# Optimization experiments

Hardware: AMD Instinct MI355X
Metric: run time of the kernel (lower is better)

Reference implementation:

```python
import jax, jax.numpy as jnp
import numpy as np

N = 50000      # nodes
E = 800000     # edges
F_IN = 500     # input features
H = 128        # hidden_channels
C = 10         # classes


def setup_inputs() -> dict:
    key = jax.random.key(0)
    ks = jax.random.split(key, 9)
    x = jax.random.normal(ks[0], (N, F_IN), dtype=jnp.float32)
    edge_index = jax.random.randint(ks[1], (2, E), 0, N, dtype=jnp.int32)
    W1 = jax.random.normal(ks[2], (F_IN, H), dtype=jnp.float32) * 0.05
    b1 = jnp.zeros((H,), dtype=jnp.float32)
    W2 = jax.random.normal(ks[3], (H, H), dtype=jnp.float32) * 0.05
    b2 = jnp.zeros((H,), dtype=jnp.float32)
    Wo = jax.random.normal(ks[4], (H, C), dtype=jnp.float32) * 0.05
    bo = jnp.zeros((C,), dtype=jnp.float32)
    return {"x": x, "edge_index": edge_index, "W1": W1, "b1": b1,
            "W2": W2, "b2": b2, "Wo": Wo, "bo": bo}


def _gcn_conv(x, src, dst, norm, W, b):
    # x: [N, F] -> [N, out]; PyG GCNConv: transform, then normalized scatter-add
    h = x @ W                                    # [N, out]
    msg = h[src] * norm[:, None]                 # [E+N, out] gathered messages
    agg = jax.ops.segment_sum(msg, dst, num_segments=N)
    return agg + b


def reference(x, edge_index, W1, b1, W2, b2, Wo, bo):
    loop = jnp.arange(N, dtype=edge_index.dtype)
    src = jnp.concatenate([edge_index[0], loop])  # add self-loops
    dst = jnp.concatenate([edge_index[1], loop])
    # symmetric normalization deg^-1/2 A_hat deg^-1/2 (deg counted at target)
    deg = jnp.zeros((N,), dtype=x.dtype).at[dst].add(1.0)
    dis = jnp.where(deg > 0, jax.lax.rsqrt(deg), 0.0)
    norm = dis[src] * dis[dst]

    h = jax.nn.relu(_gcn_conv(x, src, dst, norm, W1, b1))
    h = jax.nn.relu(_gcn_conv(h, src, dst, norm, W2, b2))
    # eval-mode: dropout is identity
    return jax.nn.softmax(h @ Wo + bo, axis=1)
```

## Files before the change

### kernel.cpp

```cpp
#include <hip/hip_runtime.h>
#include <hip/hip_bf16.h>
#include <stdint.h>

#define N_NODES 50000
#define N_EDGES 800000
#define F_IN    500
#define HID     128
#define NCLS    10

typedef __attribute__((ext_vector_type(8))) short bf16x8;
typedef __attribute__((ext_vector_type(4))) float f32x4;

__device__ __forceinline__ float bf_lo(uint32_t u) { return __uint_as_float(u << 16); }
__device__ __forceinline__ float bf_hi(uint32_t u) { return __uint_as_float(u & 0xffff0000u); }
__device__ __forceinline__ uint32_t bf_pack(float a, float b) {
    __hip_bfloat162 t; t.x = __float2bfloat16(a); t.y = __float2bfloat16(b);
    uint32_t r; __builtin_memcpy(&r, &t, 4); return r;
}


__global__ __launch_bounds__(256) void count_deg_k(const int* __restrict__ dst, int* __restrict__ cnt) {
    int e = blockIdx.x * 256 + threadIdx.x;
    if (e < N_EDGES) atomicAdd(&cnt[dst[e]], 1);
}

__global__ __launch_bounds__(1024) void scan_dis_k(const int* __restrict__ cnt,
                                                   int* __restrict__ off,
                                                   float* __restrict__ dis) {
    __shared__ int part[1024];
    const int PER = 52;
    int tid = threadIdx.x;
    int base = tid * PER;
    int vals[PER];
    #pragma unroll
    for (int i = 0; i < PER; i += 4) {
        int idx = base + i;
        int4 v = make_int4(0, 0, 0, 0);
        if (idx + 3 < N_NODES) {
            v = *(const int4*)&cnt[idx];
        } else {
            if (idx + 0 < N_NODES) v.x = cnt[idx + 0];
            if (idx + 1 < N_NODES) v.y = cnt[idx + 1];
            if (idx + 2 < N_NODES) v.z = cnt[idx + 2];
            if (idx + 3 < N_NODES) v.w = cnt[idx + 3];
        }
        vals[i + 0] = v.x; vals[i + 1] = v.y; vals[i + 2] = v.z; vals[i + 3] = v.w;
    }
    int s = 0;
    #pragma unroll
    for (int i = 0; i < PER; ++i) s += vals[i];
    part[tid] = s;
    __syncthreads();
    for (int o = 1; o < 1024; o <<= 1) {
        int v = (tid >= o) ? part[tid - o] : 0;
        __syncthreads();
        part[tid] += v;
        __syncthreads();
    }
    int run = part[tid] - s;
    #pragma unroll
    for (int i = 0; i < PER; ++i) {
        int idx = base + i;
        if (idx < N_NODES) {
            off[idx] = run; run += vals[i];
            dis[idx] = rsqrtf((float)(vals[i] + 1));
        }
    }
    if (tid == 1023) off[N_NODES] = N_EDGES;
}

__global__ __launch_bounds__(256) void fill_csr_k(const int* __restrict__ src,
                                                  const int* __restrict__ dst,
                                                  const int* __restrict__ off,
                                                  int* __restrict__ cnt,
                                                  int* __restrict__ csr) {
    int e = blockIdx.x * 256 + threadIdx.x;
    if (e < N_EDGES) {
        int d = dst[e];
        int old = atomicAdd(&cnt[d], -1);
        csr[off[d] + old - 1] = src[e];
    }
}


__global__ __launch_bounds__(256) void transpose_both_k(const float* __restrict__ W1,
                                                        const float* __restrict__ W2,
                                                        __hip_bfloat16* __restrict__ W1T,
                                                        __hip_bfloat16* __restrict__ W2T) {
    int id = blockIdx.x * 256 + threadIdx.x;
    if (id < 128 * 512) {
        int n = id >> 9, k = id & 511;
        W1T[id] = (k < F_IN) ? __float2bfloat16(W1[(long)k * 128 + n]) : __float2bfloat16(0.f);
    } else {
        int id2 = id - 128 * 512;
        if (id2 < 128 * 128) {
            int n = id2 >> 7, k = id2 & 127;
            W2T[id2] = __float2bfloat16(W2[(long)k * 128 + n]);
        }
    }
}


template<int KPAD, int KREAL, bool AF32>
__global__ __launch_bounds__(256) void gemm_mfma_k(const void* __restrict__ Av,
                                                   const __hip_bfloat16* __restrict__ BT,
                                                   __hip_bfloat16* __restrict__ Out, int M) {
    __shared__ __hip_bfloat16 smem[64 * 72 + 128 * 72];
    auto As = (__hip_bfloat16 (*)[72])smem;
    auto Bs = (__hip_bfloat16 (*)[72])(smem + 64 * 72);

    const int tid  = threadIdx.x;
    const int row0 = blockIdx.x * 64;
    const int wid  = tid >> 6, lane = tid & 63;
    const int wr   = (wid >> 1) * 32;
    const int wc   = (wid & 1) * 64;
    const int l15  = lane & 15;
    const int lk   = (lane >> 4) * 8;

    f32x4 acc[2][4];
    #pragma unroll
    for (int i = 0; i < 2; ++i)
        #pragma unroll
        for (int j = 0; j < 4; ++j) acc[i][j] = (f32x4){0.f, 0.f, 0.f, 0.f};

    const int arow = tid >> 2;
    const int aseg = (tid & 3) * 16;
    const int brow = tid >> 1;
    const int bseg = (tid & 1) * 32;
    const bool rowok = (row0 + arow) < M;

    bf16x8 a0, a1, b0, b1, b2v, b3;

    auto loadA = [&](int k0, bf16x8& r0, bf16x8& r1) {
        if (AF32) {
            const float* ap = (const float*)Av + (size_t)(row0 + arow) * KREAL + k0 + aseg;
            float v[16];
            if (rowok && (k0 + aseg + 16 <= KREAL)) {
                #pragma unroll
                for (int i = 0; i < 4; ++i) {
                    float4 f = ((const float4*)ap)[i];
                    v[4*i] = f.x; v[4*i+1] = f.y; v[4*i+2] = f.z; v[4*i+3] = f.w;
                }
            } else {
                #pragma unroll
                for (int i = 0; i < 16; ++i) {
                    int gk = k0 + aseg + i;
                    v[i] = (rowok && gk < KREAL) ? ap[i] : 0.f;
                }
            }
            __hip_bfloat16 bb[16];
            #pragma unroll
            for (int i = 0; i < 16; ++i) bb[i] = __float2bfloat16(v[i]);
            r0 = *(bf16x8*)&bb[0]; r1 = *(bf16x8*)&bb[8];
        } else {
            const __hip_bfloat16* ap = (const __hip_bfloat16*)Av + (size_t)(row0 + arow) * KREAL + k0 + aseg;
            if (rowok) { r0 = ((const bf16x8*)ap)[0]; r1 = ((const bf16x8*)ap)[1]; }
            else       { r0 = (bf16x8)(short)0;       r1 = (bf16x8)(short)0; }
        }
    };
    auto loadB = [&](int k0, bf16x8& r0, bf16x8& r1, bf16x8& r2, bf16x8& r3) {
        const __hip_bfloat16* bp = BT + (size_t)brow * KPAD + k0 + bseg;
        r0 = ((const bf16x8*)bp)[0]; r1 = ((const bf16x8*)bp)[1];
        r2 = ((const bf16x8*)bp)[2]; r3 = ((const bf16x8*)bp)[3];
    };

    loadA(0, a0, a1);
    loadB(0, b0, b1, b2v, b3);
    const int NT = KPAD / 64;
    for (int t = 0; t < NT; ++t) {
        *(bf16x8*)&As[arow][aseg]      = a0;
        *(bf16x8*)&As[arow][aseg + 8]  = a1;
        *(bf16x8*)&Bs[brow][bseg]      = b0;
        *(bf16x8*)&Bs[brow][bseg + 8]  = b1;
        *(bf16x8*)&Bs[brow][bseg + 16] = b2v;
        *(bf16x8*)&Bs[brow][bseg + 24] = b3;
        __syncthreads();
        if (t + 1 < NT) {
            loadA((t + 1) * 64, a0, a1);
            loadB((t + 1) * 64, b0, b1, b2v, b3);
        }
        #pragma unroll
        for (int kk = 0; kk < 64; kk += 32) {
            bf16x8 af[2], bfr[4];
            #pragma unroll
            for (int i = 0; i < 2; ++i)
                af[i] = *(const bf16x8*)&As[wr + i * 16 + l15][kk + lk];
            #pragma unroll
            for (int j = 0; j < 4; ++j)
                bfr[j] = *(const bf16x8*)&Bs[wc + j * 16 + l15][kk + lk];
            #pragma unroll
            for (int i = 0; i < 2; ++i)
                #pragma unroll
                for (int j = 0; j < 4; ++j)
                    acc[i][j] = __builtin_amdgcn_mfma_f32_16x16x32_bf16(af[i], bfr[j], acc[i][j], 0, 0, 0);
        }
        __syncthreads();
    }

    auto Cs = (__hip_bfloat16 (*)[136])smem;
    const int r4 = (lane >> 4) * 4;
    #pragma unroll
    for (int i = 0; i < 2; ++i)
        #pragma unroll
        for (int j = 0; j < 4; ++j)
            #pragma unroll
            for (int r = 0; r < 4; ++r)
                Cs[wr + i * 16 + r4 + r][wc + j * 16 + l15] = __float2bfloat16(acc[i][j][r]);
    __syncthreads();
    int trow = tid >> 2, tseg = (tid & 3) * 32;
    if (row0 + trow < M) {
        bf16x8* op = (bf16x8*)(Out + (size_t)(row0 + trow) * 128 + tseg);
        #pragma unroll
        for (int s = 0; s < 4; ++s) op[s] = *(bf16x8*)&Cs[trow][tseg + 8 * s];
    }
}


__global__ __launch_bounds__(256) void agg_bf16_k(const __hip_bfloat16* __restrict__ Hin,
                                                  __hip_bfloat16* __restrict__ Hout,
                                                  const int* __restrict__ off,
                                                  const int* __restrict__ csr,
                                                  const float* __restrict__ dis,
                                                  const float* __restrict__ bias) {
    int w = (blockIdx.x * 256 + threadIdx.x) >> 6;
    int lane = threadIdx.x & 63;
    if (w >= N_NODES) return;
    int e0 = off[w], e1 = off[w + 1];
    float dn = dis[w];
    const uint32_t* hrow = (const uint32_t*)Hin;

    uint32_t u = hrow[(size_t)w * 64 + lane];
    float sw = dn * dn;
    float ax = bf_lo(u) * sw, ay = bf_hi(u) * sw;

    int e = e0;
    for (; e + 4 <= e1; e += 4) {
        int s0 = csr[e], s1 = csr[e + 1], s2 = csr[e + 2], s3 = csr[e + 3];
        float w0 = dis[s0] * dn, w1 = dis[s1] * dn, w2 = dis[s2] * dn, w3 = dis[s3] * dn;
        uint32_t m0 = hrow[(size_t)s0 * 64 + lane];
        uint32_t m1 = hrow[(size_t)s1 * 64 + lane];
        uint32_t m2 = hrow[(size_t)s2 * 64 + lane];
        uint32_t m3 = hrow[(size_t)s3 * 64 + lane];
        ax = fmaf(bf_lo(m0), w0, ax); ay = fmaf(bf_hi(m0), w0, ay);
        ax = fmaf(bf_lo(m1), w1, ax); ay = fmaf(bf_hi(m1), w1, ay);
        ax = fmaf(bf_lo(m2), w2, ax); ay = fmaf(bf_hi(m2), w2, ay);
        ax = fmaf(bf_lo(m3), w3, ax); ay = fmaf(bf_hi(m3), w3, ay);
    }
    for (; e < e1; ++e) {
        int s = csr[e];
        float wgt = dis[s] * dn;
        uint32_t m = hrow[(size_t)s * 64 + lane];
        ax = fmaf(bf_lo(m), wgt, ax);
        ay = fmaf(bf_hi(m), wgt, ay);
    }
    float2 bv = ((const float2*)bias)[lane];
    float ox = fmaxf(ax + bv.x, 0.f);
    float oy = fmaxf(ay + bv.y, 0.f);
    ((uint32_t*)Hout)[(size_t)w * 64 + lane] = bf_pack(ox, oy);
}


__global__ __launch_bounds__(256) void agg_head_k(const __hip_bfloat16* __restrict__ Hin,
                                                  const int* __restrict__ off,
                                                  const int* __restrict__ csr,
                                                  const float* __restrict__ dis,
                                                  const float* __restrict__ b2,
                                                  const float* __restrict__ Wo,
                                                  const float* __restrict__ bo,
                                                  float* __restrict__ out) {
    __shared__ float wsh[HID * NCLS];
    __shared__ float bsh[NCLS];
    int tid = threadIdx.x;
    for (int i = tid; i < HID * NCLS; i += 256) wsh[i] = Wo[i];
    if (tid < NCLS) bsh[tid] = bo[tid];
    __syncthreads();

    int w = (blockIdx.x * 256 + tid) >> 6;
    int lane = tid & 63;
    if (w >= N_NODES) return;

    float wreg0[NCLS], wreg1[NCLS];
    #pragma unroll
    for (int c = 0; c < NCLS; ++c) {
        wreg0[c] = wsh[(2 * lane) * NCLS + c];
        wreg1[c] = wsh[(2 * lane + 1) * NCLS + c];
    }

    int e0 = off[w], e1 = off[w + 1];
    float dn = dis[w];
    const uint32_t* hrow = (const uint32_t*)Hin;

    uint32_t u = hrow[(size_t)w * 64 + lane];
    float sw = dn * dn;
    float ax = bf_lo(u) * sw, ay = bf_hi(u) * sw;

    int e = e0;
    for (; e + 4 <= e1; e += 4) {
        int s0 = csr[e], s1 = csr[e + 1], s2 = csr[e + 2], s3 = csr[e + 3];
        float w0 = dis[s0] * dn, w1 = dis[s1] * dn, w2 = dis[s2] * dn, w3 = dis[s3] * dn;
        uint32_t m0 = hrow[(size_t)s0 * 64 + lane];
        uint32_t m1 = hrow[(size_t)s1 * 64 + lane];
        uint32_t m2 = hrow[(size_t)s2 * 64 + lane];
        uint32_t m3 = hrow[(size_t)s3 * 64 + lane];
        ax = fmaf(bf_lo(m0), w0, ax); ay = fmaf(bf_hi(m0), w0, ay);
        ax = fmaf(bf_lo(m1), w1, ax); ay = fmaf(bf_hi(m1), w1, ay);
        ax = fmaf(bf_lo(m2), w2, ax); ay = fmaf(bf_hi(m2), w2, ay);
        ax = fmaf(bf_lo(m3), w3, ax); ay = fmaf(bf_hi(m3), w3, ay);
    }
    for (; e < e1; ++e) {
        int s = csr[e];
        float wgt = dis[s] * dn;
        uint32_t m = hrow[(size_t)s * 64 + lane];
        ax = fmaf(bf_lo(m), wgt, ax);
        ay = fmaf(bf_hi(m), wgt, ay);
    }
    float2 bv = ((const float2*)b2)[lane];
    float hx = fmaxf(ax + bv.x, 0.f);
    float hy = fmaxf(ay + bv.y, 0.f);

    float l[NCLS];
    #pragma unroll
    for (int c = 0; c < NCLS; ++c) {
        float p = fmaf(hx, wreg0[c], hy * wreg1[c]);
        #pragma unroll
        for (int o = 32; o > 0; o >>= 1) p += __shfl_xor(p, o);
        l[c] = p + bsh[c];
    }
    if (lane == 0) {
        float m = l[0];
        #pragma unroll
        for (int c = 1; c < NCLS; ++c) m = fmaxf(m, l[c]);
        float es[NCLS]; float ssum = 0.f;
        #pragma unroll
        for (int c = 0; c < NCLS; ++c) { es[c] = __expf(l[c] - m); ssum += es[c]; }
        float inv = 1.f / ssum;
        #pragma unroll
        for (int c = 0; c < NCLS; ++c) out[(size_t)w * NCLS + c] = es[c] * inv;
    }
}


static inline char* align256(char* p) {
    return (char*)(((uintptr_t)p + 255) & ~(uintptr_t)255);
}

extern "C" void kernel_launch(void* const* d_in, const int* in_sizes, int n_in,
                              void* d_out, int out_size, void* d_ws, size_t ws_size,
                              hipStream_t stream) {
    const float* x   = (const float*)d_in[0];
    const int*   ei  = (const int*)d_in[1];
    const float* W1  = (const float*)d_in[2];
    const float* b1  = (const float*)d_in[3];
    const float* W2  = (const float*)d_in[4];
    const float* b2  = (const float*)d_in[5];
    const float* Wo  = (const float*)d_in[6];
    const float* bo  = (const float*)d_in[7];
    float* out = (float*)d_out;

    const int* srcp = ei;
    const int* dstp = ei + N_EDGES;

    char* wsb = (char*)d_ws;
    __hip_bfloat16* hA = (__hip_bfloat16*)align256(wsb);  wsb = (char*)(hA + (size_t)N_NODES * HID);
    __hip_bfloat16* hB = (__hip_bfloat16*)align256(wsb);  wsb = (char*)(hB + (size_t)N_NODES * HID);
    __hip_bfloat16* W1T = (__hip_bfloat16*)align256(wsb); wsb = (char*)(W1T + 128 * 512);
    __hip_bfloat16* W2T = (__hip_bfloat16*)align256(wsb); wsb = (char*)(W2T + 128 * 128);
    int*   cnt = (int*)align256(wsb);                     wsb = (char*)(cnt + N_NODES);
    int*   off = (int*)align256(wsb);                     wsb = (char*)(off + N_NODES + 1);
    int*   csr = (int*)align256(wsb);                     wsb = (char*)(csr + N_EDGES);
    float* dis = (float*)align256(wsb);                   wsb = (char*)(dis + N_NODES);

    hipMemsetAsync(cnt, 0, sizeof(int) * N_NODES, stream);

    int ebl = (N_EDGES + 255) / 256;
    count_deg_k<<<ebl, 256, 0, stream>>>(dstp, cnt);
    scan_dis_k<<<1, 1024, 0, stream>>>(cnt, off, dis);
    fill_csr_k<<<ebl, 256, 0, stream>>>(srcp, dstp, off, cnt, csr);
    transpose_both_k<<<(128 * 512 + 128 * 128 + 255) / 256, 256, 0, stream>>>(W1, W2, W1T, W2T);

    int gblocks = (N_NODES + 63) / 64;
    int wblocks = (N_NODES + 3) / 4;

    gemm_mfma_k<512, 500, true><<<gblocks, 256, 0, stream>>>(x, W1T, hA, N_NODES);
    agg_bf16_k<<<wblocks, 256, 0, stream>>>(hA, hB, off, csr, dis, b1);
    gemm_mfma_k<128, 128, false><<<gblocks, 256, 0, stream>>>(hB, W2T, hA, N_NODES);
    agg_head_k<<<wblocks, 256, 0, stream>>>(hA, off, csr, dis, b2, Wo, bo, out);
}
```

Measured before the change: 442.0 us.

## Cooperatively load neighbor indices via shuffles, fuse transpose into scan, parallel softmax store

The aggregation kernels now have each wave load up to 64 neighbor indices and their weights at once, one per lane, and broadcast them with shuffles. Each step then issues 8 independent row gathers instead of 4 serial index-then-row loads. The weight transpose runs in extra blocks of the single-block scan kernel, which removes one launch and lets it overlap the serial scan. The softmax output is written by 10 lanes with a coalesced store instead of a serial loop in lane 0. The cost is more shuffle instructions and unused lanes in the broadcast for low-degree nodes.

```diff
diff --git a/kernel.cpp b/kernel.cpp
--- a/kernel.cpp
+++ b/kernel.cpp
@@ -24,12 +24,30 @@
     if (e < N_EDGES) atomicAdd(&cnt[dst[e]], 1);
 }
 
-__global__ __launch_bounds__(1024) void scan_dis_k(const int* __restrict__ cnt,
-                                                   int* __restrict__ off,
-                                                   float* __restrict__ dis) {
+__global__ __launch_bounds__(1024) void scan_dis_transpose_k(const int* __restrict__ cnt,
+                                                             int* __restrict__ off,
+                                                             float* __restrict__ dis,
+                                                             const float* __restrict__ W1,
+                                                             const float* __restrict__ W2,
+                                                             __hip_bfloat16* __restrict__ W1T,
+                                                             __hip_bfloat16* __restrict__ W2T) {
+    int tid = threadIdx.x;
+    if (blockIdx.x != 0) {
+        int id = (blockIdx.x - 1) * 1024 + tid;
+        if (id < 128 * 512) {
+            int n = id >> 9, k = id & 511;
+            W1T[id] = (k < F_IN) ? __float2bfloat16(W1[(long)k * 128 + n]) : __float2bfloat16(0.f);
+        } else {
+            int id2 = id - 128 * 512;
+            if (id2 < 128 * 128) {
+                int n = id2 >> 7, k = id2 & 127;
+                W2T[id2] = __float2bfloat16(W2[(long)k * 128 + n]);
+            }
+        }
+        return;
+    }
     __shared__ int part[1024];
     const int PER = 52;
-    int tid = threadIdx.x;
     int base = tid * PER;
     int vals[PER];
     #pragma unroll
@@ -79,24 +97,6 @@
         int d = dst[e];
         int old = atomicAdd(&cnt[d], -1);
         csr[off[d] + old - 1] = src[e];
-    }
-}
-
-
-__global__ __launch_bounds__(256) void transpose_both_k(const float* __restrict__ W1,
-                                                        const float* __restrict__ W2,
-                                                        __hip_bfloat16* __restrict__ W1T,
-                                                        __hip_bfloat16* __restrict__ W2T) {
-    int id = blockIdx.x * 256 + threadIdx.x;
-    if (id < 128 * 512) {
-        int n = id >> 9, k = id & 511;
-        W1T[id] = (k < F_IN) ? __float2bfloat16(W1[(long)k * 128 + n]) : __float2bfloat16(0.f);
-    } else {
-        int id2 = id - 128 * 512;
-        if (id2 < 128 * 128) {
-            int n = id2 >> 7, k = id2 & 127;
-            W2T[id2] = __float2bfloat16(W2[(long)k * 128 + n]);
-        }
     }
 }
 
@@ -216,6 +216,37 @@
 }
 
 
+__device__ __forceinline__ void agg_core(const uint32_t* __restrict__ hrow,
+                                         const int* __restrict__ csr,
+                                         const float* __restrict__ dis,
+                                         int e0, int e1, int lane, float dn,
+                                         float& ax, float& ay) {
+    int deg = e1 - e0;
+    for (int base = 0; base < deg; base += 64) {
+        int nb = min(64, deg - base);
+        int sl = 0; float wl = 0.f;
+        if (lane < nb) {
+            sl = csr[e0 + base + lane];
+            wl = dis[sl] * dn;
+        }
+        for (int j = 0; j < nb; j += 8) {
+            uint32_t m[8]; float ww[8];
+            #pragma unroll
+            for (int k = 0; k < 8; ++k) {
+                int   sk = __shfl(sl, j + k);
+                float wk = __shfl(wl, j + k);
+                m[k]  = hrow[(size_t)sk * 64 + lane];
+                ww[k] = wk;
+            }
+            #pragma unroll
+            for (int k = 0; k < 8; ++k) {
+                ax = fmaf(bf_lo(m[k]), ww[k], ax);
+                ay = fmaf(bf_hi(m[k]), ww[k], ay);
+            }
+        }
+    }
+}
+
 __global__ __launch_bounds__(256) void agg_bf16_k(const __hip_bfloat16* __restrict__ Hin,
                                                   __hip_bfloat16* __restrict__ Hout,
                                                   const int* __restrict__ off,
@@ -233,26 +264,8 @@
     float sw = dn * dn;
     float ax = bf_lo(u) * sw, ay = bf_hi(u) * sw;
 
-    int e = e0;
-    for (; e + 4 <= e1; e += 4) {
-        int s0 = csr[e], s1 = csr[e + 1], s2 = csr[e + 2], s3 = csr[e + 3];
-        float w0 = dis[s0] * dn, w1 = dis[s1] * dn, w2 = dis[s2] * dn, w3 = dis[s3] * dn;
-        uint32_t m0 = hrow[(size_t)s0 * 64 + lane];
-        uint32_t m1 = hrow[(size_t)s1 * 64 + lane];
-        uint32_t m2 = hrow[(size_t)s2 * 64 + lane];
-        uint32_t m3 = hrow[(size_t)s3 * 64 + lane];
-        ax = fmaf(bf_lo(m0), w0, ax); ay = fmaf(bf_hi(m0), w0, ay);
-        ax = fmaf(bf_lo(m1), w1, ax); ay = fmaf(bf_hi(m1), w1, ay);
-        ax = fmaf(bf_lo(m2), w2, ax); ay = fmaf(bf_hi(m2), w2, ay);
-        ax = fmaf(bf_lo(m3), w3, ax); ay = fmaf(bf_hi(m3), w3, ay);
-    }
-    for (; e < e1; ++e) {
-        int s = csr[e];
-        float wgt = dis[s] * dn;
-        uint32_t m = hrow[(size_t)s * 64 + lane];
-        ax = fmaf(bf_lo(m), wgt, ax);
-        ay = fmaf(bf_hi(m), wgt, ay);
-    }
+    agg_core(hrow, csr, dis, e0, e1, lane, dn, ax, ay);
+
     float2 bv = ((const float2*)bias)[lane];
     float ox = fmaxf(ax + bv.x, 0.f);
     float oy = fmaxf(ay + bv.y, 0.f);
@@ -294,26 +307,8 @@
     float sw = dn * dn;
     float ax = bf_lo(u) * sw, ay = bf_hi(u) * sw;
 
-    int e = e0;
-    for (; e + 4 <= e1; e += 4) {
-        int s0 = csr[e], s1 = csr[e + 1], s2 = csr[e + 2], s3 = csr[e + 3];
-        float w0 = dis[s0] * dn, w1 = dis[s1] * dn, w2 = dis[s2] * dn, w3 = dis[s3] * dn;
-        uint32_t m0 = hrow[(size_t)s0 * 64 + lane];
-        uint32_t m1 = hrow[(size_t)s1 * 64 + lane];
-        uint32_t m2 = hrow[(size_t)s2 * 64 + lane];
-        uint32_t m3 = hrow[(size_t)s3 * 64 + lane];
-        ax = fmaf(bf_lo(m0), w0, ax); ay = fmaf(bf_hi(m0), w0, ay);
-        ax = fmaf(bf_lo(m1), w1, ax); ay = fmaf(bf_hi(m1), w1, ay);
-        ax = fmaf(bf_lo(m2), w2, ax); ay = fmaf(bf_hi(m2), w2, ay);
-        ax = fmaf(bf_lo(m3), w3, ax); ay = fmaf(bf_hi(m3), w3, ay);
-    }
-    for (; e < e1; ++e) {
-        int s = csr[e];
-        float wgt = dis[s] * dn;
-        uint32_t m = hrow[(size_t)s * 64 + lane];
-        ax = fmaf(bf_lo(m), wgt, ax);
-        ay = fmaf(bf_hi(m), wgt, ay);
-    }
+    agg_core(hrow, csr, dis, e0, e1, lane, dn, ax, ay);
+
     float2 bv = ((const float2*)b2)[lane];
     float hx = fmaxf(ax + bv.x, 0.f);
     float hy = fmaxf(ay + bv.y, 0.f);
@@ -326,17 +321,17 @@
         for (int o = 32; o > 0; o >>= 1) p += __shfl_xor(p, o);
         l[c] = p + bsh[c];
     }
-    if (lane == 0) {
-        float m = l[0];
-        #pragma unroll
-        for (int c = 1; c < NCLS; ++c) m = fmaxf(m, l[c]);
-        float es[NCLS]; float ssum = 0.f;
-        #pragma unroll
-        for (int c = 0; c < NCLS; ++c) { es[c] = __expf(l[c] - m); ssum += es[c]; }
-        float inv = 1.f / ssum;
-        #pragma unroll
-        for (int c = 0; c < NCLS; ++c) out[(size_t)w * NCLS + c] = es[c] * inv;
-    }
+    float m = l[0];
+    #pragma unroll
+    for (int c = 1; c < NCLS; ++c) m = fmaxf(m, l[c]);
+    float es[NCLS]; float ssum = 0.f;
+    #pragma unroll
+    for (int c = 0; c < NCLS; ++c) { es[c] = __expf(l[c] - m); ssum += es[c]; }
+    float inv = 1.f / ssum;
+    float vout = 0.f;
+    #pragma unroll
+    for (int c = 0; c < NCLS; ++c) vout = (lane == c) ? es[c] * inv : vout;
+    if (lane < NCLS) out[(size_t)w * NCLS + lane] = vout;
 }
 
 
@@ -374,9 +369,8 @@
 
     int ebl = (N_EDGES + 255) / 256;
     count_deg_k<<<ebl, 256, 0, stream>>>(dstp, cnt);
-    scan_dis_k<<<1, 1024, 0, stream>>>(cnt, off, dis);
+    scan_dis_transpose_k<<<81, 1024, 0, stream>>>(cnt, off, dis, W1, W2, W1T, W2T);
     fill_csr_k<<<ebl, 256, 0, stream>>>(srcp, dstp, off, cnt, csr);
-    transpose_both_k<<<(128 * 512 + 128 * 128 + 255) / 256, 256, 0, stream>>>(W1, W2, W1T, W2T);
 
     int gblocks = (N_NODES + 63) / 64;
     int wblocks = (N_NODES + 3) / 4;
```

After: 432.5 us. 1.02x faster.
